# Optimization experiments

Hardware: AMD Instinct MI355X
Metric: run time of the kernel (lower is better)

## Reference

```python
import jax, jax.numpy as jnp
import numpy as np

D_MODEL = 1024
NUM_HEADS = 16
D_K = 1024
D_V = 1024
D_IN = 1024
THETA = 10000.0
B, S = 2, 2048


def setup_inputs() -> dict:
    key = jax.random.key(0)
    k1, k2, k3, k4, k5 = jax.random.split(key, 5)
    std_qkv = (2.0 / (D_IN + D_K)) ** 0.5
    std_o = (2.0 / (D_V + D_MODEL)) ** 0.5
    x = jax.random.normal(k1, (B, S, D_IN), jnp.float32)
    wq = jax.random.normal(k2, (D_IN, D_K), jnp.float32) * std_qkv
    wk = jax.random.normal(k3, (D_IN, D_K), jnp.float32) * std_qkv
    wv = jax.random.normal(k4, (D_IN, D_V), jnp.float32) * std_qkv
    wo = jax.random.normal(k5, (D_V, D_MODEL), jnp.float32) * std_o
    return {"x": x, "wq": wq, "wk": wk, "wv": wv, "wo": wo}


def _rope(t, theta):
    # t: (H, B, S, hd) -- interleaved-pair RoPE, angles pos * theta^(-2i/hd)
    hd = t.shape[-1]
    inv_freq = 1.0 / (theta ** (jnp.arange(0, hd, 2, dtype=jnp.float32) / hd))  # (hd/2,)
    pos = jnp.arange(t.shape[-2], dtype=jnp.float32)
    ang = pos[:, None] * inv_freq[None, :]                                       # (S, hd/2)
    cos, sin = jnp.cos(ang), jnp.sin(ang)
    tp = t.reshape(t.shape[:-1] + (hd // 2, 2))
    t0, t1 = tp[..., 0], tp[..., 1]
    out = jnp.stack([t0 * cos - t1 * sin, t0 * sin + t1 * cos], axis=-1)
    return out.reshape(t.shape)


def reference(x, wq, wk, wv, wo):
    b, s, _ = x.shape
    hd = D_K // NUM_HEADS
    hdv = D_V // NUM_HEADS
    # fused QKV proj (math identical to concat-then-matmul)
    q = jnp.einsum('bsd,de->bse', x, wq).reshape(b, s, NUM_HEADS, hd).transpose(2, 0, 1, 3)
    k = jnp.einsum('bsd,de->bse', x, wk).reshape(b, s, NUM_HEADS, hd).transpose(2, 0, 1, 3)
    v = jnp.einsum('bsd,de->bse', x, wv).reshape(b, s, NUM_HEADS, hdv).transpose(2, 0, 1, 3)
    q = _rope(q, THETA)
    k = _rope(k, THETA)
    scale = 1.0 / jnp.sqrt(jnp.asarray(hd, jnp.float32))
    scores = jnp.einsum('hbqd,hbkd->hbqk', q, k) * scale                 # (H,B,S,S)
    causal = jnp.tril(jnp.ones((s, s), dtype=bool))
    scores = jnp.where(causal, scores, -jnp.inf)
    attn = jax.nn.softmax(scores, axis=-1)
    o = jnp.einsum('hbqk,hbkd->hbqd', attn, v)                            # (H,B,S,hdv)
    o = o.transpose(1, 2, 0, 3).reshape(b, s, D_V)                        # merge heads (outer)
    return jnp.einsum('bsd,de->bse', o, wo)
```

## Files before the change

### kernel.cpp

```cpp
#include <hip/hip_runtime.h>
#include <stdint.h>

typedef __attribute__((ext_vector_type(8))) short short8;
typedef __attribute__((ext_vector_type(4))) float f32x4;
typedef __attribute__((ext_vector_type(4))) unsigned short ushort4v;
typedef __attribute__((ext_vector_type(2))) unsigned int uint2v;

static __device__ __forceinline__ unsigned short f2b(float f) {
  union { float f; unsigned int u; } v; v.f = f;
  unsigned int r = v.u + 0x7FFFu + ((v.u >> 16) & 1u);
  return (unsigned short)(r >> 16);
}

static __device__ __forceinline__ float exp2fast(float x) {
#if __has_builtin(__builtin_amdgcn_exp2f)
  return __builtin_amdgcn_exp2f(x);
#else
  return exp2f(x);
#endif
}

static __device__ __forceinline__ unsigned int cvtpk(float lo, float hi) {
  unsigned int r;
  asm("v_cvt_pk_bf16_f32 %0, %1, %2" : "=v"(r) : "v"(lo), "v"(hi));
  return r;
}

static __device__ __forceinline__ float xor16max(float x) {
#if __has_builtin(__builtin_amdgcn_permlane16_swap)
  unsigned u = __float_as_uint(x);
  uint2v r = __builtin_amdgcn_permlane16_swap(u, u, false, false);
  return fmaxf(__uint_as_float(r[0]), __uint_as_float(r[1]));
#else
  return fmaxf(x, __shfl_xor(x, 16));
#endif
}
static __device__ __forceinline__ float xor32max(float x) {
#if __has_builtin(__builtin_amdgcn_permlane32_swap)
  unsigned u = __float_as_uint(x);
  uint2v r = __builtin_amdgcn_permlane32_swap(u, u, false, false);
  return fmaxf(__uint_as_float(r[0]), __uint_as_float(r[1]));
#else
  return fmaxf(x, __shfl_xor(x, 32));
#endif
}
static __device__ __forceinline__ float xor16add(float x) {
#if __has_builtin(__builtin_amdgcn_permlane16_swap)
  unsigned u = __float_as_uint(x);
  uint2v r = __builtin_amdgcn_permlane16_swap(u, u, false, false);
  return __uint_as_float(r[0]) + __uint_as_float(r[1]);
#else
  return x + __shfl_xor(x, 16);
#endif
}
static __device__ __forceinline__ float xor32add(float x) {
#if __has_builtin(__builtin_amdgcn_permlane32_swap)
  unsigned u = __float_as_uint(x);
  uint2v r = __builtin_amdgcn_permlane32_swap(u, u, false, false);
  return __uint_as_float(r[0]) + __uint_as_float(r[1]);
#else
  return x + __shfl_xor(x, 32);
#endif
}

static __device__ __forceinline__ void gload16(const void* g, void* l) {
  __builtin_amdgcn_global_load_lds(
      (const __attribute__((address_space(1))) unsigned int*)g,
      (__attribute__((address_space(3))) unsigned int*)l, 16, 0, 0);
}


__global__ __launch_bounds__(256) void cast_x_kernel(const float* __restrict__ x,
                                                     unsigned short* __restrict__ xb) {
  int i = (blockIdx.x * 256 + threadIdx.x) * 4;
  float4 v = *(const float4*)(x + i);
  ushort4v o = { f2b(v.x), f2b(v.y), f2b(v.z), f2b(v.w) };
  *(ushort4v*)(xb + i) = o;
}

__global__ __launch_bounds__(256) void transpose_cast_kernel(
    const float* __restrict__ wq, const float* __restrict__ wk,
    const float* __restrict__ wv, const float* __restrict__ wo,
    unsigned short* __restrict__ wT) {
  const int z = blockIdx.z;
  const float* src = (z == 0) ? wq : (z == 1) ? wk : (z == 2) ? wv : wo;
  unsigned short* dst = wT + (size_t)z * 1048576;
  __shared__ float t[32][33];
  const int tid = threadIdx.x;
  const int tx = tid & 31, ty = tid >> 5;
  const int n0 = blockIdx.x * 32, k0 = blockIdx.y * 32;
#pragma unroll
  for (int i = 0; i < 4; ++i) {
    int r = ty + i * 8;
    t[r][tx] = src[(size_t)(k0 + r) * 1024 + n0 + tx];
  }
  __syncthreads();
#pragma unroll
  for (int i = 0; i < 4; ++i) {
    int r = ty + i * 8;
    dst[(size_t)(n0 + r) * 1024 + k0 + tx] = f2b(t[tx][r]);
  }
}

__global__ __launch_bounds__(256) void rope_tab_kernel(float* __restrict__ ct,
                                                       float* __restrict__ st) {
  int i = blockIdx.x * 256 + threadIdx.x;
  int s = i >> 5, p = i & 31;
  float ang = (float)s * powf(10000.0f, -(float)(2 * p) / 64.0f);
  ct[i] = cosf(ang);
  st[i] = sinf(ang);
}


__global__ __launch_bounds__(256) void gemm_kernel(
    const unsigned short* __restrict__ A, const unsigned short* __restrict__ WT,
    unsigned short* __restrict__ Qb, unsigned short* __restrict__ Kb,
    unsigned short* __restrict__ VTb, float* __restrict__ Fout,
    const float* __restrict__ ctab, const float* __restrict__ stab, int finalMode) {
  __shared__ unsigned short As[128 * 32];
  __shared__ unsigned short Bs[128 * 32];
  const int tid = threadIdx.x;
  const int w = tid >> 6, lane = tid & 63;
  const int m0 = blockIdx.x * 128, n0 = blockIdx.y * 128;
  int mode;
  const unsigned short* Bt;
  if (finalMode) { mode = 3; Bt = WT; }
  else { mode = blockIdx.z; Bt = WT + (size_t)mode * 1048576; }
  const int wr = w >> 1, wc = w & 1;
  const int srow = lane >> 2, scol = lane & 3;
  f32x4 acc[4][4] = {};
  for (int k0 = 0; k0 < 1024; k0 += 32) {
#pragma unroll
    for (int c = 0; c < 2; ++c) {
      int chunk = w * 2 + c;
      gload16(A + (size_t)(m0 + chunk * 16 + srow) * 1024 + k0 + scol * 8,
              (char*)As + chunk * 1024);
      gload16(Bt + (size_t)(n0 + chunk * 16 + srow) * 1024 + k0 + scol * 8,
              (char*)Bs + chunk * 1024);
    }
    __syncthreads();
    short8 af[4], bf[4];
#pragma unroll
    for (int i = 0; i < 4; ++i) {
      af[i] = *(const short8*)((const char*)As +
              ((wr * 64 + i * 16 + (lane & 15)) * 64 + (lane >> 4) * 16));
      bf[i] = *(const short8*)((const char*)Bs +
              ((wc * 64 + i * 16 + (lane & 15)) * 64 + (lane >> 4) * 16));
    }
#pragma unroll
    for (int i = 0; i < 4; ++i)
#pragma unroll
      for (int j = 0; j < 4; ++j)
        acc[i][j] = __builtin_amdgcn_mfma_f32_16x16x32_bf16(af[i], bf[j], acc[i][j], 0, 0, 0);
    __syncthreads();
  }

  if (mode < 2) {
    unsigned short* dst = mode ? Kb : Qb;
    const float qscale = mode ? 1.0f : 0.125f * 1.44269504088896f;
#pragma unroll
    for (int i = 0; i < 4; ++i) {
#pragma unroll
      for (int j = 0; j < 4; ++j) {
        int n = n0 + wc * 64 + j * 16 + (lane & 15);
        int h = n >> 6, d = n & 63;
        int pairIdx = d >> 1;
        bool even = (n & 1) == 0;
#pragma unroll
        for (int r = 0; r < 4; ++r) {
          int m = m0 + wr * 64 + i * 16 + (lane >> 4) * 4 + r;
          int b = m >> 11, s = m & 2047;
          float v = acc[i][j][r];
          float pv = __shfl_xor(v, 1);
          float c = ctab[s * 32 + pairIdx], sn = stab[s * 32 + pairIdx];
          float ov = (even ? (v * c - pv * sn) : (pv * sn + v * c)) * qscale;
          dst[(size_t)((h * 2 + b) * 2048 + s) * 64 + d] = f2b(ov);
        }
      }
    }
  } else if (mode == 2) {
#pragma unroll
    for (int i = 0; i < 4; ++i) {
#pragma unroll
      for (int j = 0; j < 4; ++j) {
        int n = n0 + wc * 64 + j * 16 + (lane & 15);
        int h = n >> 6, d = n & 63;
        int mBase = m0 + wr * 64 + i * 16 + (lane >> 4) * 4;
        int b = mBase >> 11, s = mBase & 2047;
        ushort4v pk = { f2b(acc[i][j][0]), f2b(acc[i][j][1]),
                        f2b(acc[i][j][2]), f2b(acc[i][j][3]) };
        *(ushort4v*)(VTb + (size_t)((h * 2 + b) * 64 + d) * 2048 + s) = pk;
      }
    }
  } else {
#pragma unroll
    for (int i = 0; i < 4; ++i)
#pragma unroll
      for (int j = 0; j < 4; ++j) {
        int n = n0 + wc * 64 + j * 16 + (lane & 15);
#pragma unroll
        for (int r = 0; r < 4; ++r) {
          int m = m0 + wr * 64 + i * 16 + (lane >> 4) * 4 + r;
          Fout[(size_t)m * 1024 + n] = acc[i][j][r];
        }
      }
  }
}


__device__ __forceinline__ void proc_tile(
    const short8 aq[2], const unsigned short* Ksb, const unsigned short* Vsb,
    char* Psw, int lq, int lh, int wq16, bool diag,
    float& m, float& ls, f32x4* o) {
  const int swq = (lq & 7) << 4;
  f32x4 sacc[4] = {};
  __builtin_amdgcn_s_setprio(1);
#pragma unroll
  for (int ct = 0; ct < 4; ++ct) {
    const char* base = (const char*)Ksb + (ct * 16 + lq) * 128;
#pragma unroll
    for (int half = 0; half < 2; ++half) {
      short8 ak = *(const short8*)(base + ((half * 64 + lh * 16) ^ swq));
      sacc[ct] = __builtin_amdgcn_mfma_f32_16x16x32_bf16(ak, aq[half], sacc[ct], 0, 0, 0);
    }
  }
  __builtin_amdgcn_s_setprio(0);

  if (diag) {
    int rel = wq16 + lq - 4 * lh;
#pragma unroll
    for (int ct = 0; ct < 4; ++ct)
#pragma unroll
      for (int r = 0; r < 4; ++r)
        if (ct * 16 + r > rel) sacc[ct][r] = -__builtin_inff();
  }

  float mx0 = fmaxf(fmaxf(sacc[0][0], sacc[0][1]), fmaxf(sacc[0][2], sacc[0][3]));
  float mx1 = fmaxf(fmaxf(sacc[1][0], sacc[1][1]), fmaxf(sacc[1][2], sacc[1][3]));
  float mx2 = fmaxf(fmaxf(sacc[2][0], sacc[2][1]), fmaxf(sacc[2][2], sacc[2][3]));
  float mx3 = fmaxf(fmaxf(sacc[3][0], sacc[3][1]), fmaxf(sacc[3][2], sacc[3][3]));
  float mx = fmaxf(fmaxf(mx0, mx1), fmaxf(mx2, mx3));
  mx = xor16max(mx);
  mx = xor32max(mx);
  float nm = fmaxf(m, mx);
  float al = exp2fast(m - nm);
  m = nm;
  float ps = 0.f;
#pragma unroll
  for (int ct = 0; ct < 4; ++ct)
#pragma unroll
    for (int r = 0; r < 4; ++r) {
      float p = exp2fast(sacc[ct][r] - nm);
      sacc[ct][r] = p;
      ps += p;
    }
  ls = ls * al + ps;
#pragma unroll
  for (int ct = 0; ct < 4; ++ct)
#pragma unroll
    for (int r = 0; r < 4; ++r) o[ct][r] *= al;

#pragma unroll
  for (int ct = 0; ct < 4; ++ct) {
    uint2v pk = { cvtpk(sacc[ct][0], sacc[ct][1]), cvtpk(sacc[ct][2], sacc[ct][3]) };
    *(uint2v*)(Psw + lq * 128 + ((ct * 32 + lh * 8) ^ swq)) = pk;
  }
  __builtin_amdgcn_wave_barrier();
  short8 pa[2];
#pragma unroll
  for (int half = 0; half < 2; ++half)
    pa[half] = *(const short8*)(Psw + lq * 128 + ((half * 64 + lh * 16) ^ swq));

  __builtin_amdgcn_s_setprio(1);
#pragma unroll
  for (int ct = 0; ct < 4; ++ct) {
    const char* base = (const char*)Vsb + (ct * 16 + lq) * 128;
#pragma unroll
    for (int half = 0; half < 2; ++half) {
      short8 av = *(const short8*)(base + ((half * 64 + lh * 16) ^ swq));
      o[ct] = __builtin_amdgcn_mfma_f32_16x16x32_bf16(av, pa[half], o[ct], 0, 0, 0);
    }
  }
  __builtin_amdgcn_s_setprio(0);
}

__device__ __forceinline__ void store_o(
    const f32x4* o, float ls, char* Psw, unsigned short* __restrict__ Ob,
    int lane, int lq, int lh, int w, int qb, int h, int b) {
  float l = xor32add(xor16add(ls));
  float invl = 1.0f / l;
#pragma unroll
  for (int ct = 0; ct < 4; ++ct)
#pragma unroll
    for (int r = 0; r < 4; ++r) {
      int d = ct * 16 + lh * 4 + r;
      *(unsigned short*)(Psw + lq * 128 + ((2 * d) ^ ((lq & 7) << 4))) =
          f2b(o[ct][r] * invl);
    }
  __builtin_amdgcn_wave_barrier();
#pragma unroll
  for (int pass = 0; pass < 2; ++pass) {
    int q2 = pass * 8 + (lane >> 3), d0 = (lane & 7) * 8;
    short8 vrow = *(const short8*)(Psw + q2 * 128 + ((2 * d0) ^ ((q2 & 7) << 4)));
    int s = qb + w * 16 + q2;
    *(short8*)(Ob + ((size_t)(b * 2048 + s)) * 1024 + h * 64 + d0) = vrow;
  }
}

__global__ __launch_bounds__(256) void attn_kernel(
    const unsigned short* __restrict__ Qb, const unsigned short* __restrict__ Kb,
    const unsigned short* __restrict__ VTb, unsigned short* __restrict__ Ob) {
  __shared__ unsigned short Ks[2][64 * 64];
  __shared__ unsigned short Vs[2][64 * 64];
  __shared__ unsigned short Ps[4 * 16 * 64];
  const int tid = threadIdx.x, w = tid >> 6, lane = tid & 63;
  const int bx = blockIdx.x;
  const int qt = (bx < 16) ? bx : 47 - bx;
  const int hb = blockIdx.y;
  const int h = hb >> 1, b = hb & 1;
  const unsigned short* Qhb = Qb + (size_t)hb * 2048 * 64;
  const unsigned short* Khb = Kb + (size_t)hb * 2048 * 64;
  const unsigned short* Vhb = VTb + (size_t)hb * 64 * 2048;
  char* Psw = (char*)Ps + w * 2048;
  const int lq = lane & 15, lh = lane >> 4;
  const int wq16 = w * 16;

  short8 aq[2];
  {
    int row = qt * 64 + wq16 + lq;
#pragma unroll
    for (int half = 0; half < 2; ++half)
      aq[half] = *(const short8*)(Qhb + (size_t)row * 64 + half * 32 + lh * 8);
  }
  float m = -__builtin_inff(), ls = 0.f;
  f32x4 oacc[4] = {};

  const int r0 = tid >> 3, f0 = tid & 7;
  const int so0 = r0 * 128 + ((f0 * 16) ^ ((r0 & 7) << 4));
  short8 gK[2], gV[2];
  gK[0] = *(const short8*)(Khb + (size_t)r0 * 64 + f0 * 8);
  gK[1] = *(const short8*)(Khb + (size_t)(r0 + 32) * 64 + f0 * 8);
  gV[0] = *(const short8*)(Vhb + (size_t)r0 * 2048 + f0 * 8);
  gV[1] = *(const short8*)(Vhb + (size_t)(r0 + 32) * 2048 + f0 * 8);
  *(short8*)((char*)Ks[0] + so0) = gK[0];
  *(short8*)((char*)Ks[0] + so0 + 32 * 128) = gK[1];
  *(short8*)((char*)Vs[0] + so0) = gV[0];
  *(short8*)((char*)Vs[0] + so0 + 32 * 128) = gV[1];
  __syncthreads();

  for (int kt = 0; kt <= qt; ++kt) {
    const int cur = kt & 1;
    if (kt < qt) {
      int kk0 = (kt + 1) * 64;
      gK[0] = *(const short8*)(Khb + (size_t)(kk0 + r0) * 64 + f0 * 8);
      gK[1] = *(const short8*)(Khb + (size_t)(kk0 + r0 + 32) * 64 + f0 * 8);
      gV[0] = *(const short8*)(Vhb + (size_t)r0 * 2048 + kk0 + f0 * 8);
      gV[1] = *(const short8*)(Vhb + (size_t)(r0 + 32) * 2048 + kk0 + f0 * 8);
    }
    proc_tile(aq, Ks[cur], Vs[cur], Psw, lq, lh, wq16, kt == qt, m, ls, oacc);
    if (kt < qt) {
      *(short8*)((char*)Ks[cur ^ 1] + so0) = gK[0];
      *(short8*)((char*)Ks[cur ^ 1] + so0 + 32 * 128) = gK[1];
      *(short8*)((char*)Vs[cur ^ 1] + so0) = gV[0];
      *(short8*)((char*)Vs[cur ^ 1] + so0 + 32 * 128) = gV[1];
    }
    __syncthreads();
  }

  store_o(oacc, ls, Psw, Ob, lane, lq, lh, w, qt * 64, h, b);
}


extern "C" void kernel_launch(void* const* d_in, const int* in_sizes, int n_in,
                              void* d_out, int out_size, void* d_ws, size_t ws_size,
                              hipStream_t stream) {
  const float* x  = (const float*)d_in[0];
  const float* wq = (const float*)d_in[1];
  const float* wk = (const float*)d_in[2];
  const float* wv = (const float*)d_in[3];
  const float* wo = (const float*)d_in[4];
  float* out = (float*)d_out;

  char* ws = (char*)d_ws;
  const size_t SZ = 8388608;
  unsigned short* xb  = (unsigned short*)(ws);
  unsigned short* wT  = (unsigned short*)(ws + SZ);
  unsigned short* Qb  = (unsigned short*)(ws + 2 * SZ);
  unsigned short* Kb  = (unsigned short*)(ws + 3 * SZ);
  unsigned short* VTb = (unsigned short*)(ws + 4 * SZ);
  unsigned short* Ob  = (unsigned short*)(ws + 5 * SZ);
  float* ctab = (float*)(ws + 6 * SZ);
  float* stab = (float*)(ws + 6 * SZ + 262144);
  if (ws_size < 6 * SZ + 2 * 262144) return;

  cast_x_kernel<<<4096, 256, 0, stream>>>(x, xb);
  transpose_cast_kernel<<<dim3(32, 32, 4), 256, 0, stream>>>(wq, wk, wv, wo, wT);
  rope_tab_kernel<<<256, 256, 0, stream>>>(ctab, stab);
  gemm_kernel<<<dim3(32, 8, 3), 256, 0, stream>>>(xb, wT, Qb, Kb, VTb, nullptr, ctab, stab, 0);
  attn_kernel<<<dim3(32, 32), 256, 0, stream>>>(Qb, Kb, VTb, Ob);
  gemm_kernel<<<dim3(32, 8, 1), 256, 0, stream>>>(Ob, wT + 3 * 1048576, Qb, Kb, VTb, out,
                                                  ctab, stab, 1);
}
```

Baseline: 148.5 us.

## Rewrite attention with 32x32x16 MFMA, 128-row query tiles and register P reuse

The attention kernel now gives each wave 32 query rows and uses 32x32x16 bf16 MFMAs in place of 16x16x32. Each block covers a 128-row query tile, so K/V tiles loaded into LDS serve twice as many queries and the grid is halved. P is rearranged in registers with permlane32_swap to become the B operand of the PV MFMA, removing the LDS round trip for P. The block-to-tile mapping for causal balancing also changes, with an XOR by head-batch index. The risks are higher register pressure, fewer blocks to fill the CUs, and waves idling on causal tiles they skip.

```diff
diff --git a/kernel.cpp b/kernel.cpp
--- a/kernel.cpp
+++ b/kernel.cpp
@@ -3,6 +3,7 @@
 
 typedef __attribute__((ext_vector_type(8))) short short8;
 typedef __attribute__((ext_vector_type(4))) float f32x4;
+typedef __attribute__((ext_vector_type(16))) float f32x16;
 typedef __attribute__((ext_vector_type(4))) unsigned short ushort4v;
 typedef __attribute__((ext_vector_type(2))) unsigned int uint2v;
 
@@ -26,15 +27,6 @@
   return r;
 }
 
-static __device__ __forceinline__ float xor16max(float x) {
-#if __has_builtin(__builtin_amdgcn_permlane16_swap)
-  unsigned u = __float_as_uint(x);
-  uint2v r = __builtin_amdgcn_permlane16_swap(u, u, false, false);
-  return fmaxf(__uint_as_float(r[0]), __uint_as_float(r[1]));
-#else
-  return fmaxf(x, __shfl_xor(x, 16));
-#endif
-}
 static __device__ __forceinline__ float xor32max(float x) {
 #if __has_builtin(__builtin_amdgcn_permlane32_swap)
   unsigned u = __float_as_uint(x);
@@ -42,15 +34,6 @@
   return fmaxf(__uint_as_float(r[0]), __uint_as_float(r[1]));
 #else
   return fmaxf(x, __shfl_xor(x, 32));
-#endif
-}
-static __device__ __forceinline__ float xor16add(float x) {
-#if __has_builtin(__builtin_amdgcn_permlane16_swap)
-  unsigned u = __float_as_uint(x);
-  uint2v r = __builtin_amdgcn_permlane16_swap(u, u, false, false);
-  return __uint_as_float(r[0]) + __uint_as_float(r[1]);
-#else
-  return x + __shfl_xor(x, 16);
 #endif
 }
 static __device__ __forceinline__ float xor32add(float x) {
@@ -208,132 +191,32 @@
 }
 
 
-__device__ __forceinline__ void proc_tile(
-    const short8 aq[2], const unsigned short* Ksb, const unsigned short* Vsb,
-    char* Psw, int lq, int lh, int wq16, bool diag,
-    float& m, float& ls, f32x4* o) {
-  const int swq = (lq & 7) << 4;
-  f32x4 sacc[4] = {};
-  __builtin_amdgcn_s_setprio(1);
-#pragma unroll
-  for (int ct = 0; ct < 4; ++ct) {
-    const char* base = (const char*)Ksb + (ct * 16 + lq) * 128;
-#pragma unroll
-    for (int half = 0; half < 2; ++half) {
-      short8 ak = *(const short8*)(base + ((half * 64 + lh * 16) ^ swq));
-      sacc[ct] = __builtin_amdgcn_mfma_f32_16x16x32_bf16(ak, aq[half], sacc[ct], 0, 0, 0);
-    }
-  }
-  __builtin_amdgcn_s_setprio(0);
-
-  if (diag) {
-    int rel = wq16 + lq - 4 * lh;
-#pragma unroll
-    for (int ct = 0; ct < 4; ++ct)
-#pragma unroll
-      for (int r = 0; r < 4; ++r)
-        if (ct * 16 + r > rel) sacc[ct][r] = -__builtin_inff();
-  }
-
-  float mx0 = fmaxf(fmaxf(sacc[0][0], sacc[0][1]), fmaxf(sacc[0][2], sacc[0][3]));
-  float mx1 = fmaxf(fmaxf(sacc[1][0], sacc[1][1]), fmaxf(sacc[1][2], sacc[1][3]));
-  float mx2 = fmaxf(fmaxf(sacc[2][0], sacc[2][1]), fmaxf(sacc[2][2], sacc[2][3]));
-  float mx3 = fmaxf(fmaxf(sacc[3][0], sacc[3][1]), fmaxf(sacc[3][2], sacc[3][3]));
-  float mx = fmaxf(fmaxf(mx0, mx1), fmaxf(mx2, mx3));
-  mx = xor16max(mx);
-  mx = xor32max(mx);
-  float nm = fmaxf(m, mx);
-  float al = exp2fast(m - nm);
-  m = nm;
-  float ps = 0.f;
-#pragma unroll
-  for (int ct = 0; ct < 4; ++ct)
-#pragma unroll
-    for (int r = 0; r < 4; ++r) {
-      float p = exp2fast(sacc[ct][r] - nm);
-      sacc[ct][r] = p;
-      ps += p;
-    }
-  ls = ls * al + ps;
-#pragma unroll
-  for (int ct = 0; ct < 4; ++ct)
-#pragma unroll
-    for (int r = 0; r < 4; ++r) o[ct][r] *= al;
-
-#pragma unroll
-  for (int ct = 0; ct < 4; ++ct) {
-    uint2v pk = { cvtpk(sacc[ct][0], sacc[ct][1]), cvtpk(sacc[ct][2], sacc[ct][3]) };
-    *(uint2v*)(Psw + lq * 128 + ((ct * 32 + lh * 8) ^ swq)) = pk;
-  }
-  __builtin_amdgcn_wave_barrier();
-  short8 pa[2];
-#pragma unroll
-  for (int half = 0; half < 2; ++half)
-    pa[half] = *(const short8*)(Psw + lq * 128 + ((half * 64 + lh * 16) ^ swq));
-
-  __builtin_amdgcn_s_setprio(1);
-#pragma unroll
-  for (int ct = 0; ct < 4; ++ct) {
-    const char* base = (const char*)Vsb + (ct * 16 + lq) * 128;
-#pragma unroll
-    for (int half = 0; half < 2; ++half) {
-      short8 av = *(const short8*)(base + ((half * 64 + lh * 16) ^ swq));
-      o[ct] = __builtin_amdgcn_mfma_f32_16x16x32_bf16(av, pa[half], o[ct], 0, 0, 0);
-    }
-  }
-  __builtin_amdgcn_s_setprio(0);
-}
-
-__device__ __forceinline__ void store_o(
-    const f32x4* o, float ls, char* Psw, unsigned short* __restrict__ Ob,
-    int lane, int lq, int lh, int w, int qb, int h, int b) {
-  float l = xor32add(xor16add(ls));
-  float invl = 1.0f / l;
-#pragma unroll
-  for (int ct = 0; ct < 4; ++ct)
-#pragma unroll
-    for (int r = 0; r < 4; ++r) {
-      int d = ct * 16 + lh * 4 + r;
-      *(unsigned short*)(Psw + lq * 128 + ((2 * d) ^ ((lq & 7) << 4))) =
-          f2b(o[ct][r] * invl);
-    }
-  __builtin_amdgcn_wave_barrier();
-#pragma unroll
-  for (int pass = 0; pass < 2; ++pass) {
-    int q2 = pass * 8 + (lane >> 3), d0 = (lane & 7) * 8;
-    short8 vrow = *(const short8*)(Psw + q2 * 128 + ((2 * d0) ^ ((q2 & 7) << 4)));
-    int s = qb + w * 16 + q2;
-    *(short8*)(Ob + ((size_t)(b * 2048 + s)) * 1024 + h * 64 + d0) = vrow;
-  }
-}
-
 __global__ __launch_bounds__(256) void attn_kernel(
     const unsigned short* __restrict__ Qb, const unsigned short* __restrict__ Kb,
     const unsigned short* __restrict__ VTb, unsigned short* __restrict__ Ob) {
   __shared__ unsigned short Ks[2][64 * 64];
   __shared__ unsigned short Vs[2][64 * 64];
-  __shared__ unsigned short Ps[4 * 16 * 64];
   const int tid = threadIdx.x, w = tid >> 6, lane = tid & 63;
-  const int bx = blockIdx.x;
-  const int qt = (bx < 16) ? bx : 47 - bx;
+  const int lq = lane & 31, hi = lane >> 5;
   const int hb = blockIdx.y;
+  const int bxx = blockIdx.x ^ ((hb >> 4) << 3);
+  const int qt = (bxx < 8) ? bxx : 23 - bxx;
   const int h = hb >> 1, b = hb & 1;
   const unsigned short* Qhb = Qb + (size_t)hb * 2048 * 64;
   const unsigned short* Khb = Kb + (size_t)hb * 2048 * 64;
   const unsigned short* Vhb = VTb + (size_t)hb * 64 * 2048;
-  char* Psw = (char*)Ps + w * 2048;
-  const int lq = lane & 15, lh = lane >> 4;
-  const int wq16 = w * 16;
-
-  short8 aq[2];
-  {
-    int row = qt * 64 + wq16 + lq;
-#pragma unroll
-    for (int half = 0; half < 2; ++half)
-      aq[half] = *(const short8*)(Qhb + (size_t)row * 64 + half * 32 + lh * 8);
-  }
+  const int qbase = qt * 128 + w * 32;
+  const int swq = (lq & 7) << 4;
+  const int ktmax = 2 * qt + 1;
+
+  short8 qf[4];
+#pragma unroll
+  for (int s = 0; s < 4; ++s)
+    qf[s] = *(const short8*)(Qhb + (size_t)(qbase + lq) * 64 + s * 16 + hi * 8);
+
+  const f32x16 Z16 = {0,0,0,0,0,0,0,0,0,0,0,0,0,0,0,0};
+  f32x16 o0 = Z16, o1 = Z16;
   float m = -__builtin_inff(), ls = 0.f;
-  f32x4 oacc[4] = {};
 
   const int r0 = tid >> 3, f0 = tid & 7;
   const int so0 = r0 * 128 + ((f0 * 16) ^ ((r0 & 7) << 4));
@@ -348,17 +231,87 @@
   *(short8*)((char*)Vs[0] + so0 + 32 * 128) = gV[1];
   __syncthreads();
 
-  for (int kt = 0; kt <= qt; ++kt) {
+  for (int kt = 0; kt <= ktmax; ++kt) {
     const int cur = kt & 1;
-    if (kt < qt) {
+    if (kt < ktmax) {
       int kk0 = (kt + 1) * 64;
       gK[0] = *(const short8*)(Khb + (size_t)(kk0 + r0) * 64 + f0 * 8);
       gK[1] = *(const short8*)(Khb + (size_t)(kk0 + r0 + 32) * 64 + f0 * 8);
       gV[0] = *(const short8*)(Vhb + (size_t)r0 * 2048 + kk0 + f0 * 8);
       gV[1] = *(const short8*)(Vhb + (size_t)(r0 + 32) * 2048 + kk0 + f0 * 8);
     }
-    proc_tile(aq, Ks[cur], Vs[cur], Psw, lq, lh, wq16, kt == qt, m, ls, oacc);
-    if (kt < qt) {
+    if (kt * 64 <= qbase + 31) {
+      const unsigned short* Ksb = Ks[cur];
+      const unsigned short* Vsb = Vs[cur];
+      f32x16 s0 = Z16, s1 = Z16;
+      __builtin_amdgcn_s_setprio(1);
+#pragma unroll
+      for (int st = 0; st < 4; ++st) {
+        short8 a0 = *(const short8*)((const char*)Ksb + lq * 128 +
+                    ((st * 32 + hi * 16) ^ swq));
+        short8 a1 = *(const short8*)((const char*)Ksb + (32 + lq) * 128 +
+                    ((st * 32 + hi * 16) ^ swq));
+        s0 = __builtin_amdgcn_mfma_f32_32x32x16_bf16(a0, qf[st], s0, 0, 0, 0);
+        s1 = __builtin_amdgcn_mfma_f32_32x32x16_bf16(a1, qf[st], s1, 0, 0, 0);
+      }
+      __builtin_amdgcn_s_setprio(0);
+
+      if (kt * 64 + 63 > qbase) {
+        int relk = qbase + lq - kt * 64;
+#pragma unroll
+        for (int r = 0; r < 16; ++r) {
+          int km = (r & 3) + 8 * (r >> 2) + 4 * hi;
+          if (km > relk) s0[r] = -__builtin_inff();
+          if (km + 32 > relk) s1[r] = -__builtin_inff();
+        }
+      }
+
+      float mx = s0[0];
+#pragma unroll
+      for (int r = 1; r < 16; ++r) mx = fmaxf(mx, s0[r]);
+#pragma unroll
+      for (int r = 0; r < 16; ++r) mx = fmaxf(mx, s1[r]);
+      mx = xor32max(mx);
+      float nm = fmaxf(m, mx);
+      float al = exp2fast(m - nm);
+      m = nm;
+      float ps = 0.f;
+#pragma unroll
+      for (int r = 0; r < 16; ++r) { float p = exp2fast(s0[r] - nm); s0[r] = p; ps += p; }
+#pragma unroll
+      for (int r = 0; r < 16; ++r) { float p = exp2fast(s1[r] - nm); s1[r] = p; ps += p; }
+      ls = ls * al + ps;
+      o0 *= al;
+      o1 *= al;
+
+      unsigned int pk0[8], pk1[8];
+#pragma unroll
+      for (int jp = 0; jp < 8; ++jp) {
+        pk0[jp] = cvtpk(s0[2 * jp], s0[2 * jp + 1]);
+        pk1[jp] = cvtpk(s1[2 * jp], s1[2 * jp + 1]);
+      }
+      __builtin_amdgcn_s_setprio(1);
+#pragma unroll
+      for (int ks = 0; ks < 4; ++ks) {
+        const int off = 4 * (ks & 1);
+        unsigned int a0 = (ks < 2) ? pk0[off + 0] : pk1[off + 0];
+        unsigned int a1 = (ks < 2) ? pk0[off + 1] : pk1[off + 1];
+        unsigned int b0 = (ks < 2) ? pk0[off + 2] : pk1[off + 2];
+        unsigned int b1 = (ks < 2) ? pk0[off + 3] : pk1[off + 3];
+        uint2v w0 = __builtin_amdgcn_permlane32_swap(a0, b0, false, false);
+        uint2v w1 = __builtin_amdgcn_permlane32_swap(a1, b1, false, false);
+        union { unsigned int u[4]; short8 s; } F;
+        F.u[0] = w0[0]; F.u[1] = w1[0]; F.u[2] = w0[1]; F.u[3] = w1[1];
+        short8 v0 = *(const short8*)((const char*)Vsb + lq * 128 +
+                    ((ks * 32 + hi * 16) ^ swq));
+        short8 v1 = *(const short8*)((const char*)Vsb + (32 + lq) * 128 +
+                    ((ks * 32 + hi * 16) ^ swq));
+        o0 = __builtin_amdgcn_mfma_f32_32x32x16_bf16(v0, F.s, o0, 0, 0, 0);
+        o1 = __builtin_amdgcn_mfma_f32_32x32x16_bf16(v1, F.s, o1, 0, 0, 0);
+      }
+      __builtin_amdgcn_s_setprio(0);
+    }
+    if (kt < ktmax) {
       *(short8*)((char*)Ks[cur ^ 1] + so0) = gK[0];
       *(short8*)((char*)Ks[cur ^ 1] + so0 + 32 * 128) = gK[1];
       *(short8*)((char*)Vs[cur ^ 1] + so0) = gV[0];
@@ -367,7 +320,27 @@
     __syncthreads();
   }
 
-  store_o(oacc, ls, Psw, Ob, lane, lq, lh, w, qt * 64, h, b);
+  ls = xor32add(ls);
+  float invl = 1.0f / ls;
+  char* Osw = (char*)Ks + w * 4096;
+#pragma unroll
+  for (int jp = 0; jp < 8; ++jp) {
+    const int r = 2 * jp;
+    const int km = (r & 3) + 8 * (r >> 2) + 4 * hi;
+    unsigned int pa = cvtpk(o0[r] * invl, o0[r + 1] * invl);
+    unsigned int pb = cvtpk(o1[r] * invl, o1[r + 1] * invl);
+    *(unsigned int*)(Osw + lq * 128 + ((2 * km) ^ swq)) = pa;
+    *(unsigned int*)(Osw + lq * 128 + ((2 * (km + 32)) ^ swq)) = pb;
+  }
+  __builtin_amdgcn_wave_barrier();
+#pragma unroll
+  for (int pass = 0; pass < 4; ++pass) {
+    int q2 = pass * 8 + (lane >> 3);
+    int c16 = (lane & 7) * 16;
+    short8 vrow = *(const short8*)(Osw + q2 * 128 + (c16 ^ ((q2 & 7) << 4)));
+    int srow = qbase + q2;
+    *(short8*)(Ob + (size_t)(b * 2048 + srow) * 1024 + h * 64 + (lane & 7) * 8) = vrow;
+  }
 }
 
 
@@ -397,7 +370,7 @@
   transpose_cast_kernel<<<dim3(32, 32, 4), 256, 0, stream>>>(wq, wk, wv, wo, wT);
   rope_tab_kernel<<<256, 256, 0, stream>>>(ctab, stab);
   gemm_kernel<<<dim3(32, 8, 3), 256, 0, stream>>>(xb, wT, Qb, Kb, VTb, nullptr, ctab, stab, 0);
-  attn_kernel<<<dim3(32, 32), 256, 0, stream>>>(Qb, Kb, VTb, Ob);
+  attn_kernel<<<dim3(16, 32), 256, 0, stream>>>(Qb, Kb, VTb, Ob);
   gemm_kernel<<<dim3(32, 8, 1), 256, 0, stream>>>(Ob, wT + 3 * 1048576, Qb, Kb, VTb, out,
                                                   ctab, stab, 1);
 }
```

Measured after the change: 138.9 us. 1.07x faster.
